# Kernel optimization log

Hardware: AMD Instinct MI355X
Metric: run time of the kernel (lower is better)

Reference implementation:

```python
import jax, jax.numpy as jnp
import numpy as np

N_NODES = 100000
N_EDGES = 6400000


def setup_inputs() -> dict:
    key = jax.random.key(0)
    k1, k2, k3, k4 = jax.random.split(key, 4)
    x = jax.random.normal(k1, (N_NODES, 1), dtype=jnp.float32)
    edge_index = jax.random.randint(k2, (2, N_EDGES), 0, N_NODES, dtype=jnp.int64)
    W1 = jax.random.normal(k3, (16, 1), dtype=jnp.float32) * 0.5
    b1 = jnp.zeros((16,), dtype=jnp.float32)
    W2 = jax.random.normal(k4, (2, 16), dtype=jnp.float32) * 0.25
    b2 = jnp.zeros((2,), dtype=jnp.float32)
    return {"x": x, "edge_index": edge_index, "W1": W1, "b1": b1, "W2": W2, "b2": b2}


def _gcn_norm(edge_index, num_nodes):
    # PyG gcn_norm with add_self_loops=True, edge_weight=1:
    # deg computed at target (col); norm = deg^-1/2[row] * deg^-1/2[col]
    loops = jnp.arange(num_nodes, dtype=edge_index.dtype)
    row = jnp.concatenate([edge_index[0], loops])
    col = jnp.concatenate([edge_index[1], loops])
    deg = jax.ops.segment_sum(jnp.ones(row.shape[0], dtype=jnp.float32), col,
                              num_segments=num_nodes)
    deg_inv_sqrt = jnp.where(deg > 0, jax.lax.rsqrt(deg), 0.0)
    norm = deg_inv_sqrt[row] * deg_inv_sqrt[col]
    return row, col, norm


def _gcn_conv(x, W, b, row, col, norm, num_nodes):
    h = x @ W.T                                   # [N, out]
    msg = norm[:, None] * h[row]                  # gather + scale, [E+N, out]
    out = jax.ops.segment_sum(msg, col, num_segments=num_nodes)  # scatter-add
    return out + b


def reference(x, edge_index, W1, b1, W2, b2):
    num_nodes = x.shape[0]
    row, col, norm = _gcn_norm(edge_index, num_nodes)
    h = _gcn_conv(x, W1, b1, row, col, norm, num_nodes)
    h = jax.nn.relu(h)
    out = _gcn_conv(h, W2, b2, row, col, norm, num_nodes)
    return out
```

## Files before the change

kernel.cpp:

```cpp
#include <hip/hip_runtime.h>
#include <cmath>


static constexpr int CSH   = 11;
static constexpr int CW    = 1 << CSH;
static constexpr int MAXNC = 64;
static constexpr int NB1   = 512;

__host__ __device__ __forceinline__ int chunk_of(int e) {
    return ((e + NB1 * 4 - 1) / (NB1 * 4)) * 4;
}

__global__ __launch_bounds__(256) void k_scatter(const int* __restrict__ row,
        const int* __restrict__ col, int* __restrict__ P1, int* __restrict__ CNT,
        int e, int NC, int PAD) {
    __shared__ int cur[MAXNC];
    const int b = blockIdx.x, tid = threadIdx.x;
    for (int j = tid; j < NC; j += 256) cur[j] = 0;
    __syncthreads();
    const int chunk = chunk_of(e);
    const int lo = b * chunk, end = min(lo + chunk, e);
    const size_t rbase = (size_t)b * NC * PAD;
    for (int i0 = lo + tid * 4; i0 + 3 < end; i0 += 1024) {
        int4 c4 = *reinterpret_cast<const int4*>(col + i0);
        int4 r4 = *reinterpret_cast<const int4*>(row + i0);
        int ca[4] = {c4.x, c4.y, c4.z, c4.w};
        int ra[4] = {r4.x, r4.y, r4.z, r4.w};
#pragma unroll
        for (int m = 0; m < 4; ++m) {
            int k = ca[m] >> CSH;
            int pos = atomicAdd(&cur[k], 1);
            if (pos < PAD)
                P1[rbase + (size_t)k * PAD + pos] = (ra[m] << CSH) | (ca[m] & (CW - 1));
        }
    }
    const int tailStart = lo + ((end - lo) & ~3);
    for (int i = tailStart + tid; i < end; i += 256) {
        int c = col[i], r = row[i];
        int k = c >> CSH;
        int pos = atomicAdd(&cur[k], 1);
        if (pos < PAD)
            P1[rbase + (size_t)k * PAD + pos] = (r << CSH) | (c & (CW - 1));
    }
    __syncthreads();
    for (int j = tid; j < NC; j += 256) CNT[b * NC + j] = min(cur[j], PAD);
}

__global__ __launch_bounds__(512) void k_deg(const int* __restrict__ P1,
        const int* __restrict__ CNT, int* __restrict__ Pd, int NC, int C, int PAD) {
    __shared__ __align__(16) int bin[CW];
    const int k = blockIdx.x / C, j = blockIdx.x % C;
    const int tid = threadIdx.x, wave = tid >> 6, lane = tid & 63;
    for (int q = tid; q < CW; q += 512) bin[q] = 0;
    __syncthreads();
    const int b0 = (j * NB1) / C, b1 = ((j + 1) * NB1) / C;
    for (int b = b0 + wave; b < b1; b += 8) {
        const int cnt = CNT[b * NC + k];
        const int* seg = P1 + ((size_t)b * NC + k) * PAD;
        const int nv = cnt & ~3;
        for (int i = lane * 4; i < nv; i += 256) {
            int4 a = *reinterpret_cast<const int4*>(seg + i);
            atomicAdd(&bin[a.x & (CW - 1)], 1); atomicAdd(&bin[a.y & (CW - 1)], 1);
            atomicAdd(&bin[a.z & (CW - 1)], 1); atomicAdd(&bin[a.w & (CW - 1)], 1);
        }
        for (int i = nv + lane; i < cnt; i += 64)
            atomicAdd(&bin[seg[i] & (CW - 1)], 1);
    }
    __syncthreads();
    int4* o4 = reinterpret_cast<int4*>(Pd + ((size_t)k * C + j) * CW);
    const int4* b4 = reinterpret_cast<const int4*>(bin);
    for (int q = tid; q < CW / 4; q += 512) o4[q] = b4[q];
}

__global__ __launch_bounds__(512) void k_aggf(const int* __restrict__ P1,
        const int* __restrict__ CNT, const float* __restrict__ src,
        float* __restrict__ Pf, int NC, int C, int PAD) {
    __shared__ __align__(16) float bin[CW];
    const int k = blockIdx.x / C, j = blockIdx.x % C;
    const int tid = threadIdx.x, wave = tid >> 6, lane = tid & 63;
    for (int q = tid; q < CW; q += 512) bin[q] = 0.0f;
    __syncthreads();
    const int b0 = (j * NB1) / C, b1 = ((j + 1) * NB1) / C;
    for (int b = b0 + wave; b < b1; b += 8) {
        const int cnt = CNT[b * NC + k];
        const int* seg = P1 + ((size_t)b * NC + k) * PAD;
        const int nv = cnt & ~3;
        for (int i = lane * 4; i < nv; i += 256) {
            int4 a = *reinterpret_cast<const int4*>(seg + i);
            float v0 = src[a.x >> CSH], v1 = src[a.y >> CSH];
            float v2 = src[a.z >> CSH], v3 = src[a.w >> CSH];
            atomicAdd(&bin[a.x & (CW - 1)], v0); atomicAdd(&bin[a.y & (CW - 1)], v1);
            atomicAdd(&bin[a.z & (CW - 1)], v2); atomicAdd(&bin[a.w & (CW - 1)], v3);
        }
        for (int i = nv + lane; i < cnt; i += 64) {
            int p = seg[i];
            atomicAdd(&bin[p & (CW - 1)], src[p >> CSH]);
        }
    }
    __syncthreads();
    float4* o4 = reinterpret_cast<float4*>(Pf + ((size_t)k * C + j) * CW);
    const float4* b4 = reinterpret_cast<const float4*>(bin);
    for (int q = tid; q < CW / 4; q += 512) o4[q] = b4[q];
}

__device__ __forceinline__ unsigned long long pack_u(float2 uv) {
    float cx = fminf(fmaxf(uv.x, -15.9f), 15.9f);
    float cy = fminf(fmaxf(uv.y, -15.9f), 15.9f);
    unsigned int tx = (unsigned int)__float2int_rn(fmaf(cx, 524288.0f, 8388608.0f));
    unsigned int ty = (unsigned int)__float2int_rn(fmaf(cy, 524288.0f, 8388608.0f));
    return ((unsigned long long)ty << 32) | tx;
}

__global__ __launch_bounds__(512) void k_agg2f(const int* __restrict__ P1,
        const int* __restrict__ CNT, const float2* __restrict__ u,
        unsigned long long* __restrict__ Pq, int NC, int C, int PAD) {
    __shared__ unsigned long long bin[CW];
    const int k = blockIdx.x / C, j = blockIdx.x % C;
    const int tid = threadIdx.x, wave = tid >> 6, lane = tid & 63;
    for (int q = tid; q < CW; q += 512) bin[q] = 0ull;
    __syncthreads();
    const int b0 = (j * NB1) / C, b1 = ((j + 1) * NB1) / C;
    for (int b = b0 + wave; b < b1; b += 8) {
        const int cnt = CNT[b * NC + k];
        const int* seg = P1 + ((size_t)b * NC + k) * PAD;
        const int nv = cnt & ~3;
        for (int i = lane * 4; i < nv; i += 256) {
            int4 a = *reinterpret_cast<const int4*>(seg + i);
            unsigned long long q0 = pack_u(u[a.x >> CSH]);
            unsigned long long q1 = pack_u(u[a.y >> CSH]);
            unsigned long long q2 = pack_u(u[a.z >> CSH]);
            unsigned long long q3 = pack_u(u[a.w >> CSH]);
            atomicAdd(&bin[a.x & (CW - 1)], q0); atomicAdd(&bin[a.y & (CW - 1)], q1);
            atomicAdd(&bin[a.z & (CW - 1)], q2); atomicAdd(&bin[a.w & (CW - 1)], q3);
        }
        for (int i = nv + lane; i < cnt; i += 64) {
            int p = seg[i];
            atomicAdd(&bin[p & (CW - 1)], pack_u(u[p >> CSH]));
        }
    }
    __syncthreads();
    unsigned long long* o = Pq + ((size_t)k * C + j) * CW;
    for (int q = tid; q < CW; q += 512) o[q] = bin[q];
}

__global__ void k_prep(const int* __restrict__ Pd, const float* __restrict__ x,
        float* __restrict__ dis, float* __restrict__ t, float* __restrict__ degf,
        int n, int C) {
    int c = blockIdx.x * blockDim.x + threadIdx.x;
    if (c >= n) return;
    int k = c >> CSH, l = c & (CW - 1);
    int d = 0;
    for (int j = 0; j < C; ++j) d += Pd[((size_t)k * C + j) * CW + l];
    degf[c] = (float)d;
    float di = rsqrtf(1.0f + (float)d);
    dis[c] = di;
    t[c] = di * x[c];
}

__global__ void k_mlp(const float* __restrict__ Pf, const float* __restrict__ dis,
        const float* __restrict__ t, const float* __restrict__ W1,
        const float* __restrict__ b1, const float* __restrict__ W2,
        float2* __restrict__ u, int n, int C) {
    int c = blockIdx.x * blockDim.x + threadIdx.x;
    if (c >= n) return;
    int k = c >> CSH, l = c & (CW - 1);
    float S = 0.0f;
    for (int j = 0; j < C; ++j) S += Pf[((size_t)k * C + j) * CW + l];
    float di = dis[c];
    float s = di * (S + t[c]);
    float a0 = 0.0f, a1 = 0.0f;
#pragma unroll
    for (int j = 0; j < 16; ++j) {
        float hh = fmaxf(fmaf(s, W1[j], b1[j]), 0.0f);
        a0 = fmaf(W2[j],      hh, a0);
        a1 = fmaf(W2[16 + j], hh, a1);
    }
    u[c] = make_float2(di * a0, di * a1);
}

__global__ void k_out(const unsigned long long* __restrict__ Pq,
        const float* __restrict__ dis, const float* __restrict__ degf,
        const float2* __restrict__ u, const float* __restrict__ b2,
        float2* __restrict__ out, int n, int C) {
    int c = blockIdx.x * blockDim.x + threadIdx.x;
    if (c >= n) return;
    int k = c >> CSH, l = c & (CW - 1);
    unsigned long long S = 0ull;
    for (int j = 0; j < C; ++j) S += Pq[((size_t)k * C + j) * CW + l];
    double dg = (double)degf[c] * 8388608.0;
    double sx = ((double)(unsigned int)(S & 0xffffffffULL) - dg) * (1.0 / 524288.0);
    double sy = ((double)(unsigned int)(S >> 32)            - dg) * (1.0 / 524288.0);
    float di = dis[c];
    float2 uc = u[c];
    out[c] = make_float2(b2[0] + di * ((float)sx + uc.x),
                         b2[1] + di * ((float)sy + uc.y));
}

__global__ void f_init_deg(float* deg, int n) {
    int i = blockIdx.x * blockDim.x + threadIdx.x;
    if (i < n) deg[i] = 1.0f;
}
__global__ void f_deg(const int* col, float* deg, int e) {
    int i = blockIdx.x * blockDim.x + threadIdx.x;
    if (i < e) atomicAdd(&deg[col[i]], 1.0f);
}
__global__ void f_dis_self(const float* x, float* deg_dis, float* s, int n) {
    int i = blockIdx.x * blockDim.x + threadIdx.x;
    if (i < n) { float di = rsqrtf(deg_dis[i]); deg_dis[i] = di; s[i] = di * di * x[i]; }
}
__global__ void f_agg1(const int* row, const int* col, const float* dis,
                       const float* x, float* s, int e) {
    int i = blockIdx.x * blockDim.x + threadIdx.x;
    if (i < e) { int r = row[i], c = col[i]; atomicAdd(&s[c], dis[r] * dis[c] * x[r]); }
}
__global__ void f_mlp(const float* s, const float* dis, const float* W1,
                      const float* b1, const float* W2, const float* b2,
                      float* h2, float* out, int n) {
    int i = blockIdx.x * blockDim.x + threadIdx.x;
    if (i < n) {
        float sv = s[i], a0 = 0.0f, a1 = 0.0f;
#pragma unroll
        for (int j = 0; j < 16; ++j) {
            float h1 = fmaxf(sv * W1[j] + b1[j], 0.0f);
            a0 = fmaf(W2[j], h1, a0); a1 = fmaf(W2[16 + j], h1, a1);
        }
        h2[2 * i] = a0; h2[2 * i + 1] = a1;
        float d2 = dis[i] * dis[i];
        out[2 * i] = b2[0] + d2 * a0; out[2 * i + 1] = b2[1] + d2 * a1;
    }
}
__global__ void f_agg2(const int* row, const int* col, const float* dis,
                       const float* h2, float* out, int e) {
    int i = blockIdx.x * blockDim.x + threadIdx.x;
    if (i < e) {
        int r = row[i], c = col[i];
        float nm = dis[r] * dis[c];
        float2 hv = *reinterpret_cast<const float2*>(&h2[2 * r]);
        atomicAdd(&out[2 * c], nm * hv.x);
        atomicAdd(&out[2 * c + 1], nm * hv.y);
    }
}

extern "C" void kernel_launch(void* const* d_in, const int* in_sizes, int n_in,
                              void* d_out, int out_size, void* d_ws, size_t ws_size,
                              hipStream_t stream) {
    const float* x  = (const float*)d_in[0];
    const int*   ei = (const int*)d_in[1];
    const float* W1 = (const float*)d_in[2];
    const float* b1 = (const float*)d_in[3];
    const float* W2 = (const float*)d_in[4];
    const float* b2 = (const float*)d_in[5];

    const int n = in_sizes[0];
    const int e = in_sizes[1] / 2;
    const int* row = ei;
    const int* col = ei + e;

    const int NC = (n + CW - 1) >> CSH;
    const size_t NCW = (size_t)NC * CW;

    const int chunk = chunk_of(e);
    const int lam = NC > 0 ? chunk / NC : 0;
    int PAD = lam + 8 * (int)std::sqrt((double)(lam > 0 ? lam : 1)) + 32;
    PAD = (PAD + 3) & ~3;

    const size_t ws4 = ws_size / 4;
    const size_t p1sz = (size_t)NB1 * NC * PAD;
    size_t base4 = p1sz + (size_t)NB1 * NC + 5ull * (size_t)n;
    base4 = (base4 + 3) & ~(size_t)3;
    long long avail = (long long)ws4 - (long long)base4;
    int Cs = (avail > 0) ? (int)min((long long)32, avail / (long long)NCW) : 0;
    int Cv = (avail > 0) ? (int)min((long long)24, avail / (long long)(2 * NCW)) : 0;

    if (NC > MAXNC || NC < 4 || Cs < 2 || Cv < 2 ||
        (long long)e > 100ll * (long long)n) {
        float* dis = (float*)d_ws; float* s = dis + n; float* h2 = s + n;
        const int gn = (n + 255) / 256, ge = (e + 255) / 256;
        f_init_deg<<<gn, 256, 0, stream>>>(dis, n);
        f_deg<<<ge, 256, 0, stream>>>(col, dis, e);
        f_dis_self<<<gn, 256, 0, stream>>>(x, dis, s, n);
        f_agg1<<<ge, 256, 0, stream>>>(row, col, dis, x, s, e);
        f_mlp<<<gn, 256, 0, stream>>>(s, dis, W1, b1, W2, b2, h2, (float*)d_out, n);
        f_agg2<<<ge, 256, 0, stream>>>(row, col, dis, h2, (float*)d_out, e);
        return;
    }

    int*    P1   = (int*)d_ws;
    int*    CNT  = P1 + p1sz;
    float*  dis  = (float*)(CNT + (size_t)NB1 * NC);
    float*  t    = dis + n;
    float*  degf = t + n;
    float2* u    = (float2*)(degf + n);
    float*  Pp   = (float*)((char*)d_ws + base4 * 4);

    const int gn = (n + 255) / 256;

    k_scatter<<<NB1, 256, 0, stream>>>(row, col, P1, CNT, e, NC, PAD);
    k_deg    <<<NC * Cs, 512, 0, stream>>>(P1, CNT, (int*)Pp, NC, Cs, PAD);
    k_prep   <<<gn, 256, 0, stream>>>((const int*)Pp, x, dis, t, degf, n, Cs);
    k_aggf   <<<NC * Cs, 512, 0, stream>>>(P1, CNT, t, Pp, NC, Cs, PAD);
    k_mlp    <<<gn, 256, 0, stream>>>(Pp, dis, t, W1, b1, W2, u, n, Cs);
    k_agg2f  <<<NC * Cv, 512, 0, stream>>>(P1, CNT, u, (unsigned long long*)Pp, NC, Cv, PAD);
    k_out    <<<gn, 256, 0, stream>>>((const unsigned long long*)Pp, dis, degf, u, b2,
                                      (float2*)d_out, n, Cv);
}
```

Measured before the change: 227.9 us.

## Build per-destination CSR-like placement once, then gather without atomics in both layers

Adds a k_place pass that bins the already-bucketed edges into a per-block, per-destination column-major slot array (with a shared overflow spill list). It also writes per-destination counts, which k_prep reuses as the degree histogram. Both aggregation layers become gather kernels: each thread owns four destinations and sums source values sequentially, replacing LDS float atomics and the fixed-point 64-bit packing with plain float sums. The cost is an extra placement pass with scattered global writes and a larger workspace. The gathers can also suffer load imbalance when destination counts vary.

```diff
diff --git a/kernel.cpp b/kernel.cpp
--- a/kernel.cpp
+++ b/kernel.cpp
@@ -6,6 +6,7 @@
 static constexpr int CW    = 1 << CSH;
 static constexpr int MAXNC = 64;
 static constexpr int NB1   = 512;
+static constexpr int SPAD  = 4096;
 
 __host__ __device__ __forceinline__ int chunk_of(int e) {
     return ((e + NB1 * 4 - 1) / (NB1 * 4)) * 4;
@@ -46,13 +47,20 @@
     for (int j = tid; j < NC; j += 256) CNT[b * NC + j] = min(cur[j], PAD);
 }
 
-__global__ __launch_bounds__(512) void k_deg(const int* __restrict__ P1,
-        const int* __restrict__ CNT, int* __restrict__ Pd, int NC, int C, int PAD) {
-    __shared__ __align__(16) int bin[CW];
+__global__ __launch_bounds__(512) void k_place(const int* __restrict__ P1,
+        const int* __restrict__ CNT, int* __restrict__ P2, int* __restrict__ CNT2,
+        int* __restrict__ SP, int* __restrict__ SPC,
+        int NC, int C, int PAD, int NPAD) {
+    __shared__ int cur[CW];
+    __shared__ int scur;
     const int k = blockIdx.x / C, j = blockIdx.x % C;
+    const size_t r = blockIdx.x;
     const int tid = threadIdx.x, wave = tid >> 6, lane = tid & 63;
-    for (int q = tid; q < CW; q += 512) bin[q] = 0;
-    __syncthreads();
+    for (int q = tid; q < CW; q += 512) cur[q] = 0;
+    if (tid == 0) scur = 0;
+    __syncthreads();
+    int* __restrict__ p2 = P2 + r * CW * (size_t)NPAD;
+    int* __restrict__ sp = SP + r * SPAD;
     const int b0 = (j * NB1) / C, b1 = ((j + 1) * NB1) / C;
     for (int b = b0 + wave; b < b1; b += 8) {
         const int cnt = CNT[b * NC + k];
@@ -60,87 +68,98 @@
         const int nv = cnt & ~3;
         for (int i = lane * 4; i < nv; i += 256) {
             int4 a = *reinterpret_cast<const int4*>(seg + i);
-            atomicAdd(&bin[a.x & (CW - 1)], 1); atomicAdd(&bin[a.y & (CW - 1)], 1);
-            atomicAdd(&bin[a.z & (CW - 1)], 1); atomicAdd(&bin[a.w & (CW - 1)], 1);
-        }
-        for (int i = nv + lane; i < cnt; i += 64)
-            atomicAdd(&bin[seg[i] & (CW - 1)], 1);
-    }
-    __syncthreads();
-    int4* o4 = reinterpret_cast<int4*>(Pd + ((size_t)k * C + j) * CW);
-    const int4* b4 = reinterpret_cast<const int4*>(bin);
-    for (int q = tid; q < CW / 4; q += 512) o4[q] = b4[q];
-}
-
-__global__ __launch_bounds__(512) void k_aggf(const int* __restrict__ P1,
-        const int* __restrict__ CNT, const float* __restrict__ src,
-        float* __restrict__ Pf, int NC, int C, int PAD) {
-    __shared__ __align__(16) float bin[CW];
-    const int k = blockIdx.x / C, j = blockIdx.x % C;
-    const int tid = threadIdx.x, wave = tid >> 6, lane = tid & 63;
-    for (int q = tid; q < CW; q += 512) bin[q] = 0.0f;
-    __syncthreads();
-    const int b0 = (j * NB1) / C, b1 = ((j + 1) * NB1) / C;
-    for (int b = b0 + wave; b < b1; b += 8) {
-        const int cnt = CNT[b * NC + k];
-        const int* seg = P1 + ((size_t)b * NC + k) * PAD;
-        const int nv = cnt & ~3;
-        for (int i = lane * 4; i < nv; i += 256) {
-            int4 a = *reinterpret_cast<const int4*>(seg + i);
-            float v0 = src[a.x >> CSH], v1 = src[a.y >> CSH];
-            float v2 = src[a.z >> CSH], v3 = src[a.w >> CSH];
-            atomicAdd(&bin[a.x & (CW - 1)], v0); atomicAdd(&bin[a.y & (CW - 1)], v1);
-            atomicAdd(&bin[a.z & (CW - 1)], v2); atomicAdd(&bin[a.w & (CW - 1)], v3);
+            int vv[4] = {a.x, a.y, a.z, a.w};
+#pragma unroll
+            for (int m = 0; m < 4; ++m) {
+                const int v = vv[m];
+                const int l = v & (CW - 1);
+                const int pos = atomicAdd(&cur[l], 1);
+                if (pos < NPAD) p2[(size_t)pos * CW + l] = v >> CSH;
+                else { int s0 = atomicAdd(&scur, 1); if (s0 < SPAD) sp[s0] = v; }
+            }
         }
         for (int i = nv + lane; i < cnt; i += 64) {
-            int p = seg[i];
-            atomicAdd(&bin[p & (CW - 1)], src[p >> CSH]);
-        }
-    }
-    __syncthreads();
-    float4* o4 = reinterpret_cast<float4*>(Pf + ((size_t)k * C + j) * CW);
-    const float4* b4 = reinterpret_cast<const float4*>(bin);
-    for (int q = tid; q < CW / 4; q += 512) o4[q] = b4[q];
-}
-
-__device__ __forceinline__ unsigned long long pack_u(float2 uv) {
-    float cx = fminf(fmaxf(uv.x, -15.9f), 15.9f);
-    float cy = fminf(fmaxf(uv.y, -15.9f), 15.9f);
-    unsigned int tx = (unsigned int)__float2int_rn(fmaf(cx, 524288.0f, 8388608.0f));
-    unsigned int ty = (unsigned int)__float2int_rn(fmaf(cy, 524288.0f, 8388608.0f));
-    return ((unsigned long long)ty << 32) | tx;
-}
-
-__global__ __launch_bounds__(512) void k_agg2f(const int* __restrict__ P1,
-        const int* __restrict__ CNT, const float2* __restrict__ u,
-        unsigned long long* __restrict__ Pq, int NC, int C, int PAD) {
-    __shared__ unsigned long long bin[CW];
-    const int k = blockIdx.x / C, j = blockIdx.x % C;
-    const int tid = threadIdx.x, wave = tid >> 6, lane = tid & 63;
-    for (int q = tid; q < CW; q += 512) bin[q] = 0ull;
-    __syncthreads();
-    const int b0 = (j * NB1) / C, b1 = ((j + 1) * NB1) / C;
-    for (int b = b0 + wave; b < b1; b += 8) {
-        const int cnt = CNT[b * NC + k];
-        const int* seg = P1 + ((size_t)b * NC + k) * PAD;
-        const int nv = cnt & ~3;
-        for (int i = lane * 4; i < nv; i += 256) {
-            int4 a = *reinterpret_cast<const int4*>(seg + i);
-            unsigned long long q0 = pack_u(u[a.x >> CSH]);
-            unsigned long long q1 = pack_u(u[a.y >> CSH]);
-            unsigned long long q2 = pack_u(u[a.z >> CSH]);
-            unsigned long long q3 = pack_u(u[a.w >> CSH]);
-            atomicAdd(&bin[a.x & (CW - 1)], q0); atomicAdd(&bin[a.y & (CW - 1)], q1);
-            atomicAdd(&bin[a.z & (CW - 1)], q2); atomicAdd(&bin[a.w & (CW - 1)], q3);
-        }
-        for (int i = nv + lane; i < cnt; i += 64) {
-            int p = seg[i];
-            atomicAdd(&bin[p & (CW - 1)], pack_u(u[p >> CSH]));
-        }
-    }
-    __syncthreads();
-    unsigned long long* o = Pq + ((size_t)k * C + j) * CW;
-    for (int q = tid; q < CW; q += 512) o[q] = bin[q];
+            const int v = seg[i];
+            const int l = v & (CW - 1);
+            const int pos = atomicAdd(&cur[l], 1);
+            if (pos < NPAD) p2[(size_t)pos * CW + l] = v >> CSH;
+            else { int s0 = atomicAdd(&scur, 1); if (s0 < SPAD) sp[s0] = v; }
+        }
+    }
+    __syncthreads();
+    for (int q = tid; q < CW; q += 512) CNT2[r * CW + q] = cur[q];
+    if (tid == 0) SPC[r] = min(scur, SPAD);
+}
+
+__global__ __launch_bounds__(512) void k_gath1(const int* __restrict__ P2,
+        const int* __restrict__ CNT2, const int* __restrict__ SP,
+        const int* __restrict__ SPC, const float* __restrict__ t,
+        float* __restrict__ Pf, int NPAD) {
+    __shared__ float sbin[CW];
+    const size_t r = blockIdx.x;
+    const int tid = threadIdx.x;
+    for (int q = tid; q < CW; q += 512) sbin[q] = 0.0f;
+    __syncthreads();
+    const int spc = SPC[r];
+    for (int i = tid; i < spc; i += 512) {
+        const int v = SP[r * SPAD + i];
+        atomicAdd(&sbin[v & (CW - 1)], t[v >> CSH]);
+    }
+    __syncthreads();
+    const int* __restrict__ p2 = P2 + r * CW * (size_t)NPAD;
+    const int* __restrict__ cc = CNT2 + r * CW;
+    const int l0 = tid, l1 = tid + 512, l2 = tid + 1024, l3 = tid + 1536;
+    const int c0 = min(cc[l0], NPAD), c1 = min(cc[l1], NPAD);
+    const int c2 = min(cc[l2], NPAD), c3 = min(cc[l3], NPAD);
+    float S0 = sbin[l0], S1 = sbin[l1], S2 = sbin[l2], S3 = sbin[l3];
+    const int cm = max(max(c0, c1), max(c2, c3));
+    for (int p = 0; p < cm; ++p) {
+        const int* rp = p2 + (size_t)p * CW;
+        if (p < c0) S0 += t[rp[l0]];
+        if (p < c1) S1 += t[rp[l1]];
+        if (p < c2) S2 += t[rp[l2]];
+        if (p < c3) S3 += t[rp[l3]];
+    }
+    float* o = Pf + r * CW;
+    o[l0] = S0; o[l1] = S1; o[l2] = S2; o[l3] = S3;
+}
+
+__global__ __launch_bounds__(512) void k_gath2(const int* __restrict__ P2,
+        const int* __restrict__ CNT2, const int* __restrict__ SP,
+        const int* __restrict__ SPC, const float2* __restrict__ u,
+        float2* __restrict__ Pf2, int NPAD) {
+    __shared__ float sbx[CW];
+    __shared__ float sby[CW];
+    const size_t r = blockIdx.x;
+    const int tid = threadIdx.x;
+    for (int q = tid; q < CW; q += 512) { sbx[q] = 0.0f; sby[q] = 0.0f; }
+    __syncthreads();
+    const int spc = SPC[r];
+    for (int i = tid; i < spc; i += 512) {
+        const int v = SP[r * SPAD + i];
+        float2 uv = u[v >> CSH];
+        atomicAdd(&sbx[v & (CW - 1)], uv.x);
+        atomicAdd(&sby[v & (CW - 1)], uv.y);
+    }
+    __syncthreads();
+    const int* __restrict__ p2 = P2 + r * CW * (size_t)NPAD;
+    const int* __restrict__ cc = CNT2 + r * CW;
+    const int l0 = tid, l1 = tid + 512, l2 = tid + 1024, l3 = tid + 1536;
+    const int c0 = min(cc[l0], NPAD), c1 = min(cc[l1], NPAD);
+    const int c2 = min(cc[l2], NPAD), c3 = min(cc[l3], NPAD);
+    float S0x = sbx[l0], S1x = sbx[l1], S2x = sbx[l2], S3x = sbx[l3];
+    float S0y = sby[l0], S1y = sby[l1], S2y = sby[l2], S3y = sby[l3];
+    const int cm = max(max(c0, c1), max(c2, c3));
+    for (int p = 0; p < cm; ++p) {
+        const int* rp = p2 + (size_t)p * CW;
+        if (p < c0) { float2 v = u[rp[l0]]; S0x += v.x; S0y += v.y; }
+        if (p < c1) { float2 v = u[rp[l1]]; S1x += v.x; S1y += v.y; }
+        if (p < c2) { float2 v = u[rp[l2]]; S2x += v.x; S2y += v.y; }
+        if (p < c3) { float2 v = u[rp[l3]]; S3x += v.x; S3y += v.y; }
+    }
+    float2* o = Pf2 + r * CW;
+    o[l0] = make_float2(S0x, S0y); o[l1] = make_float2(S1x, S1y);
+    o[l2] = make_float2(S2x, S2y); o[l3] = make_float2(S3x, S3y);
 }
 
 __global__ void k_prep(const int* __restrict__ Pd, const float* __restrict__ x,
@@ -178,6 +197,120 @@
     u[c] = make_float2(di * a0, di * a1);
 }
 
+__global__ void k_out2(const float2* __restrict__ Pf2, const float* __restrict__ dis,
+        const float2* __restrict__ u, const float* __restrict__ b2,
+        float2* __restrict__ out, int n, int C) {
+    int c = blockIdx.x * blockDim.x + threadIdx.x;
+    if (c >= n) return;
+    int k = c >> CSH, l = c & (CW - 1);
+    float sx = 0.0f, sy = 0.0f;
+    for (int j = 0; j < C; ++j) {
+        float2 p = Pf2[((size_t)k * C + j) * CW + l];
+        sx += p.x; sy += p.y;
+    }
+    float di = dis[c];
+    float2 uc = u[c];
+    out[c] = make_float2(b2[0] + di * (sx + uc.x),
+                         b2[1] + di * (sy + uc.y));
+}
+
+__global__ __launch_bounds__(512) void k_deg(const int* __restrict__ P1,
+        const int* __restrict__ CNT, int* __restrict__ Pd, int NC, int C, int PAD) {
+    __shared__ __align__(16) int bin[CW];
+    const int k = blockIdx.x / C, j = blockIdx.x % C;
+    const int tid = threadIdx.x, wave = tid >> 6, lane = tid & 63;
+    for (int q = tid; q < CW; q += 512) bin[q] = 0;
+    __syncthreads();
+    const int b0 = (j * NB1) / C, b1 = ((j + 1) * NB1) / C;
+    for (int b = b0 + wave; b < b1; b += 8) {
+        const int cnt = CNT[b * NC + k];
+        const int* seg = P1 + ((size_t)b * NC + k) * PAD;
+        const int nv = cnt & ~3;
+        for (int i = lane * 4; i < nv; i += 256) {
+            int4 a = *reinterpret_cast<const int4*>(seg + i);
+            atomicAdd(&bin[a.x & (CW - 1)], 1); atomicAdd(&bin[a.y & (CW - 1)], 1);
+            atomicAdd(&bin[a.z & (CW - 1)], 1); atomicAdd(&bin[a.w & (CW - 1)], 1);
+        }
+        for (int i = nv + lane; i < cnt; i += 64)
+            atomicAdd(&bin[seg[i] & (CW - 1)], 1);
+    }
+    __syncthreads();
+    int4* o4 = reinterpret_cast<int4*>(Pd + ((size_t)k * C + j) * CW);
+    const int4* b4 = reinterpret_cast<const int4*>(bin);
+    for (int q = tid; q < CW / 4; q += 512) o4[q] = b4[q];
+}
+
+__global__ __launch_bounds__(512) void k_aggf(const int* __restrict__ P1,
+        const int* __restrict__ CNT, const float* __restrict__ src,
+        float* __restrict__ Pf, int NC, int C, int PAD) {
+    __shared__ __align__(16) float bin[CW];
+    const int k = blockIdx.x / C, j = blockIdx.x % C;
+    const int tid = threadIdx.x, wave = tid >> 6, lane = tid & 63;
+    for (int q = tid; q < CW; q += 512) bin[q] = 0.0f;
+    __syncthreads();
+    const int b0 = (j * NB1) / C, b1 = ((j + 1) * NB1) / C;
+    for (int b = b0 + wave; b < b1; b += 8) {
+        const int cnt = CNT[b * NC + k];
+        const int* seg = P1 + ((size_t)b * NC + k) * PAD;
+        const int nv = cnt & ~3;
+        for (int i = lane * 4; i < nv; i += 256) {
+            int4 a = *reinterpret_cast<const int4*>(seg + i);
+            float v0 = src[a.x >> CSH], v1 = src[a.y >> CSH];
+            float v2 = src[a.z >> CSH], v3 = src[a.w >> CSH];
+            atomicAdd(&bin[a.x & (CW - 1)], v0); atomicAdd(&bin[a.y & (CW - 1)], v1);
+            atomicAdd(&bin[a.z & (CW - 1)], v2); atomicAdd(&bin[a.w & (CW - 1)], v3);
+        }
+        for (int i = nv + lane; i < cnt; i += 64) {
+            int p = seg[i];
+            atomicAdd(&bin[p & (CW - 1)], src[p >> CSH]);
+        }
+    }
+    __syncthreads();
+    float4* o4 = reinterpret_cast<float4*>(Pf + ((size_t)k * C + j) * CW);
+    const float4* b4 = reinterpret_cast<const float4*>(bin);
+    for (int q = tid; q < CW / 4; q += 512) o4[q] = b4[q];
+}
+
+__device__ __forceinline__ unsigned long long pack_u(float2 uv) {
+    float cx = fminf(fmaxf(uv.x, -15.9f), 15.9f);
+    float cy = fminf(fmaxf(uv.y, -15.9f), 15.9f);
+    unsigned int tx = (unsigned int)__float2int_rn(fmaf(cx, 524288.0f, 8388608.0f));
+    unsigned int ty = (unsigned int)__float2int_rn(fmaf(cy, 524288.0f, 8388608.0f));
+    return ((unsigned long long)ty << 32) | tx;
+}
+
+__global__ __launch_bounds__(512) void k_agg2f(const int* __restrict__ P1,
+        const int* __restrict__ CNT, const float2* __restrict__ u,
+        unsigned long long* __restrict__ Pq, int NC, int C, int PAD) {
+    __shared__ unsigned long long bin[CW];
+    const int k = blockIdx.x / C, j = blockIdx.x % C;
+    const int tid = threadIdx.x, wave = tid >> 6, lane = tid & 63;
+    for (int q = tid; q < CW; q += 512) bin[q] = 0ull;
+    __syncthreads();
+    const int b0 = (j * NB1) / C, b1 = ((j + 1) * NB1) / C;
+    for (int b = b0 + wave; b < b1; b += 8) {
+        const int cnt = CNT[b * NC + k];
+        const int* seg = P1 + ((size_t)b * NC + k) * PAD;
+        const int nv = cnt & ~3;
+        for (int i = lane * 4; i < nv; i += 256) {
+            int4 a = *reinterpret_cast<const int4*>(seg + i);
+            unsigned long long q0 = pack_u(u[a.x >> CSH]);
+            unsigned long long q1 = pack_u(u[a.y >> CSH]);
+            unsigned long long q2 = pack_u(u[a.z >> CSH]);
+            unsigned long long q3 = pack_u(u[a.w >> CSH]);
+            atomicAdd(&bin[a.x & (CW - 1)], q0); atomicAdd(&bin[a.y & (CW - 1)], q1);
+            atomicAdd(&bin[a.z & (CW - 1)], q2); atomicAdd(&bin[a.w & (CW - 1)], q3);
+        }
+        for (int i = nv + lane; i < cnt; i += 64) {
+            int p = seg[i];
+            atomicAdd(&bin[p & (CW - 1)], pack_u(u[p >> CSH]));
+        }
+    }
+    __syncthreads();
+    unsigned long long* o = Pq + ((size_t)k * C + j) * CW;
+    for (int q = tid; q < CW; q += 512) o[q] = bin[q];
+}
+
 __global__ void k_out(const unsigned long long* __restrict__ Pq,
         const float* __restrict__ dis, const float* __restrict__ degf,
         const float2* __restrict__ u, const float* __restrict__ b2,
@@ -258,14 +391,62 @@
 
     const int NC = (n + CW - 1) >> CSH;
     const size_t NCW = (size_t)NC * CW;
+    const size_t ws4 = ws_size / 4;
 
     const int chunk = chunk_of(e);
     const int lam = NC > 0 ? chunk / NC : 0;
     int PAD = lam + 8 * (int)std::sqrt((double)(lam > 0 ? lam : 1)) + 32;
     PAD = (PAD + 3) & ~3;
-
-    const size_t ws4 = ws_size / 4;
     const size_t p1sz = (size_t)NB1 * NC * PAD;
+    const int gn = (n + 255) / 256;
+
+    if (NC <= MAXNC && NC >= 4 && e > 0) {
+        const int C2 = 10;
+        const size_t cells = (size_t)NC * C2 * CW;
+        const double lm = (double)e / (double)cells;
+        if (lm <= 32.0) {
+            const int na = (n + 3) & ~3;
+            const size_t fixed4 = p1sz + (size_t)NB1 * NC + 5ull * (size_t)na;
+            int cand[3];
+            cand[0] = (int)std::ceil(lm + 2.5 * std::sqrt(lm) + 6.0);
+            cand[1] = (int)std::ceil(lm + 1.2 * std::sqrt(lm) + 2.0);
+            cand[2] = (int)std::ceil(lm + 0.5 * std::sqrt(lm));
+            for (int ci = 0; ci < 3; ++ci) {
+                const int NPAD = cand[ci] > 4 ? cand[ci] : 4;
+                const size_t need = fixed4
+                                  + cells
+                                  + (size_t)NC * C2 + 64
+                                  + (size_t)NC * C2 * SPAD
+                                  + cells * (size_t)NPAD;
+                if (need > ws4 || p1sz < cells * 3) continue;
+
+                int*    P1   = (int*)d_ws;
+                int*    CNT  = P1 + p1sz;
+                float*  dis  = (float*)(CNT + (size_t)NB1 * NC);
+                float*  t    = dis + na;
+                float*  degf = t + na;
+                float2* u    = (float2*)(degf + na);
+                int*    CNT2 = (int*)d_ws + fixed4;
+                int*    SPC  = CNT2 + cells;
+                int*    SP   = SPC + (size_t)NC * C2 + 64;
+                int*    P2   = SP + (size_t)NC * C2 * SPAD;
+                float*  Pf   = (float*)P1;
+                float2* Pf2  = (float2*)(P1 + cells);
+
+                k_scatter<<<NB1, 256, 0, stream>>>(row, col, P1, CNT, e, NC, PAD);
+                k_place  <<<NC * C2, 512, 0, stream>>>(P1, CNT, P2, CNT2, SP, SPC,
+                                                       NC, C2, PAD, NPAD);
+                k_prep   <<<gn, 256, 0, stream>>>(CNT2, x, dis, t, degf, n, C2);
+                k_gath1  <<<NC * C2, 512, 0, stream>>>(P2, CNT2, SP, SPC, t, Pf, NPAD);
+                k_mlp    <<<gn, 256, 0, stream>>>(Pf, dis, t, W1, b1, W2, u, n, C2);
+                k_gath2  <<<NC * C2, 512, 0, stream>>>(P2, CNT2, SP, SPC, u, Pf2, NPAD);
+                k_out2   <<<gn, 256, 0, stream>>>(Pf2, dis, u, b2,
+                                                  (float2*)d_out, n, C2);
+                return;
+            }
+        }
+    }
+
     size_t base4 = p1sz + (size_t)NB1 * NC + 5ull * (size_t)n;
     base4 = (base4 + 3) & ~(size_t)3;
     long long avail = (long long)ws4 - (long long)base4;
@@ -275,7 +456,7 @@
     if (NC > MAXNC || NC < 4 || Cs < 2 || Cv < 2 ||
         (long long)e > 100ll * (long long)n) {
         float* dis = (float*)d_ws; float* s = dis + n; float* h2 = s + n;
-        const int gn = (n + 255) / 256, ge = (e + 255) / 256;
+        const int ge = (e + 255) / 256;
         f_init_deg<<<gn, 256, 0, stream>>>(dis, n);
         f_deg<<<ge, 256, 0, stream>>>(col, dis, e);
         f_dis_self<<<gn, 256, 0, stream>>>(x, dis, s, n);
@@ -292,8 +473,6 @@
     float*  degf = t + n;
     float2* u    = (float2*)(degf + n);
     float*  Pp   = (float*)((char*)d_ws + base4 * 4);
-
-    const int gn = (n + 255) / 256;
 
     k_scatter<<<NB1, 256, 0, stream>>>(row, col, P1, CNT, e, NC, PAD);
     k_deg    <<<NC * Cs, 512, 0, stream>>>(P1, CNT, (int*)Pp, NC, Cs, PAD);
```

Result: slower. 272.5 us (+19.6%).

## Fuse seven pipeline kernels into one cooperative persistent kernel with grid syncs

Applied to the files above, without the earlier changes.

Replaces the seven separate launches (scatter, degree count, prep, first aggregation, MLP, second aggregation, output) with one cooperative kernel of NB1 blocks that runs each stage in turn, separated by grid.sync. Work is distributed with grid-stride job loops. The aim is to cut per-kernel launch gaps and tail drain between the short stages. In exchange, blocks now use 512 threads and a shared bin sized for the largest stage, which may reduce occupancy. Grid-wide barriers are costly and all 512 blocks must be co-resident, otherwise the code falls back to the separate launches.

```diff
diff --git a/kernel.cpp b/kernel.cpp
--- a/kernel.cpp
+++ b/kernel.cpp
@@ -1,5 +1,8 @@
 #include <hip/hip_runtime.h>
+#include <hip/hip_cooperative_groups.h>
 #include <cmath>
+
+namespace cg = cooperative_groups;
 
 
 static constexpr int CSH   = 11;
@@ -9,6 +12,208 @@
 
 __host__ __device__ __forceinline__ int chunk_of(int e) {
     return ((e + NB1 * 4 - 1) / (NB1 * 4)) * 4;
+}
+
+__device__ __forceinline__ unsigned long long pack_u(float2 uv) {
+    float cx = fminf(fmaxf(uv.x, -15.9f), 15.9f);
+    float cy = fminf(fmaxf(uv.y, -15.9f), 15.9f);
+    unsigned int tx = (unsigned int)__float2int_rn(fmaf(cx, 524288.0f, 8388608.0f));
+    unsigned int ty = (unsigned int)__float2int_rn(fmaf(cy, 524288.0f, 8388608.0f));
+    return ((unsigned long long)ty << 32) | tx;
+}
+
+__global__ __launch_bounds__(512, 4) void k_fused(
+        const int* __restrict__ row, const int* __restrict__ col,
+        const float* __restrict__ x,  const float* __restrict__ W1,
+        const float* __restrict__ b1, const float* __restrict__ W2,
+        const float* __restrict__ b2,
+        int* __restrict__ P1, int* __restrict__ CNT,
+        float* __restrict__ dis, float* __restrict__ t,
+        float* __restrict__ degf, float2* __restrict__ u,
+        float* __restrict__ Pp, float2* __restrict__ out,
+        int n, int e, int NC, int PAD, int Cs, int Cv) {
+    cg::grid_group grid = cg::this_grid();
+    __shared__ __align__(16) unsigned long long binU[CW];
+    __shared__ int cur[MAXNC];
+    int*   binI = (int*)binU;
+    float* binF = (float*)binU;
+    const int tid = threadIdx.x, wave = tid >> 6, lane = tid & 63;
+
+    {
+        const int b = blockIdx.x;
+        for (int j = tid; j < NC; j += 512) cur[j] = 0;
+        __syncthreads();
+        const int chunk = chunk_of(e);
+        const int lo = b * chunk, end = min(lo + chunk, e);
+        const size_t rbase = (size_t)b * NC * PAD;
+        for (int i0 = lo + tid * 4; i0 + 3 < end; i0 += 2048) {
+            int4 c4 = *reinterpret_cast<const int4*>(col + i0);
+            int4 r4 = *reinterpret_cast<const int4*>(row + i0);
+            int ca[4] = {c4.x, c4.y, c4.z, c4.w};
+            int ra[4] = {r4.x, r4.y, r4.z, r4.w};
+#pragma unroll
+            for (int m = 0; m < 4; ++m) {
+                int k = ca[m] >> CSH;
+                int pos = atomicAdd(&cur[k], 1);
+                if (pos < PAD)
+                    P1[rbase + (size_t)k * PAD + pos] =
+                        (ra[m] << CSH) | (ca[m] & (CW - 1));
+            }
+        }
+        const int tailStart = lo + ((end - lo) & ~3);
+        for (int i = tailStart + tid; i < end; i += 512) {
+            int c = col[i], r = row[i];
+            int k = c >> CSH;
+            int pos = atomicAdd(&cur[k], 1);
+            if (pos < PAD)
+                P1[rbase + (size_t)k * PAD + pos] = (r << CSH) | (c & (CW - 1));
+        }
+        __syncthreads();
+        for (int j = tid; j < NC; j += 512) CNT[b * NC + j] = min(cur[j], PAD);
+    }
+    grid.sync();
+
+    {
+        int* Pd = (int*)Pp;
+        for (int job = blockIdx.x; job < NC * Cs; job += NB1) {
+            const int k = job / Cs, j = job % Cs;
+            for (int q = tid; q < CW; q += 512) binI[q] = 0;
+            __syncthreads();
+            const int b0 = (j * NB1) / Cs, b1e = ((j + 1) * NB1) / Cs;
+            for (int b = b0 + wave; b < b1e; b += 8) {
+                const int cnt = CNT[b * NC + k];
+                const int* seg = P1 + ((size_t)b * NC + k) * PAD;
+                const int nv = cnt & ~3;
+                for (int i = lane * 4; i < nv; i += 256) {
+                    int4 a = *reinterpret_cast<const int4*>(seg + i);
+                    atomicAdd(&binI[a.x & (CW - 1)], 1);
+                    atomicAdd(&binI[a.y & (CW - 1)], 1);
+                    atomicAdd(&binI[a.z & (CW - 1)], 1);
+                    atomicAdd(&binI[a.w & (CW - 1)], 1);
+                }
+                for (int i = nv + lane; i < cnt; i += 64)
+                    atomicAdd(&binI[seg[i] & (CW - 1)], 1);
+            }
+            __syncthreads();
+            for (int q = tid; q < CW; q += 512)
+                Pd[((size_t)k * Cs + j) * CW + q] = binI[q];
+        }
+    }
+    grid.sync();
+
+    {
+        const int* Pd = (const int*)Pp;
+        for (int c = blockIdx.x * 512 + tid; c < n; c += NB1 * 512) {
+            int k = c >> CSH, l = c & (CW - 1);
+            int d = 0;
+            for (int j = 0; j < Cs; ++j) d += Pd[((size_t)k * Cs + j) * CW + l];
+            degf[c] = (float)d;
+            float di = rsqrtf(1.0f + (float)d);
+            dis[c] = di;
+            t[c] = di * x[c];
+        }
+    }
+    grid.sync();
+
+    {
+        for (int job = blockIdx.x; job < NC * Cs; job += NB1) {
+            const int k = job / Cs, j = job % Cs;
+            for (int q = tid; q < CW; q += 512) binF[q] = 0.0f;
+            __syncthreads();
+            const int b0 = (j * NB1) / Cs, b1e = ((j + 1) * NB1) / Cs;
+            for (int b = b0 + wave; b < b1e; b += 8) {
+                const int cnt = CNT[b * NC + k];
+                const int* seg = P1 + ((size_t)b * NC + k) * PAD;
+                const int nv = cnt & ~3;
+                for (int i = lane * 4; i < nv; i += 256) {
+                    int4 a = *reinterpret_cast<const int4*>(seg + i);
+                    float v0 = t[a.x >> CSH], v1 = t[a.y >> CSH];
+                    float v2 = t[a.z >> CSH], v3 = t[a.w >> CSH];
+                    atomicAdd(&binF[a.x & (CW - 1)], v0);
+                    atomicAdd(&binF[a.y & (CW - 1)], v1);
+                    atomicAdd(&binF[a.z & (CW - 1)], v2);
+                    atomicAdd(&binF[a.w & (CW - 1)], v3);
+                }
+                for (int i = nv + lane; i < cnt; i += 64) {
+                    int p = seg[i];
+                    atomicAdd(&binF[p & (CW - 1)], t[p >> CSH]);
+                }
+            }
+            __syncthreads();
+            for (int q = tid; q < CW; q += 512)
+                Pp[((size_t)k * Cs + j) * CW + q] = binF[q];
+        }
+    }
+    grid.sync();
+
+    {
+        for (int c = blockIdx.x * 512 + tid; c < n; c += NB1 * 512) {
+            int k = c >> CSH, l = c & (CW - 1);
+            float S = 0.0f;
+            for (int j = 0; j < Cs; ++j) S += Pp[((size_t)k * Cs + j) * CW + l];
+            float di = dis[c];
+            float s = di * (S + t[c]);
+            float a0 = 0.0f, a1 = 0.0f;
+#pragma unroll
+            for (int j = 0; j < 16; ++j) {
+                float hh = fmaxf(fmaf(s, W1[j], b1[j]), 0.0f);
+                a0 = fmaf(W2[j],      hh, a0);
+                a1 = fmaf(W2[16 + j], hh, a1);
+            }
+            u[c] = make_float2(di * a0, di * a1);
+        }
+    }
+    grid.sync();
+
+    {
+        unsigned long long* Pq = (unsigned long long*)Pp;
+        for (int job = blockIdx.x; job < NC * Cv; job += NB1) {
+            const int k = job / Cv, j = job % Cv;
+            for (int q = tid; q < CW; q += 512) binU[q] = 0ull;
+            __syncthreads();
+            const int b0 = (j * NB1) / Cv, b1e = ((j + 1) * NB1) / Cv;
+            for (int b = b0 + wave; b < b1e; b += 8) {
+                const int cnt = CNT[b * NC + k];
+                const int* seg = P1 + ((size_t)b * NC + k) * PAD;
+                const int nv = cnt & ~3;
+                for (int i = lane * 4; i < nv; i += 256) {
+                    int4 a = *reinterpret_cast<const int4*>(seg + i);
+                    unsigned long long q0 = pack_u(u[a.x >> CSH]);
+                    unsigned long long q1 = pack_u(u[a.y >> CSH]);
+                    unsigned long long q2 = pack_u(u[a.z >> CSH]);
+                    unsigned long long q3 = pack_u(u[a.w >> CSH]);
+                    atomicAdd(&binU[a.x & (CW - 1)], q0);
+                    atomicAdd(&binU[a.y & (CW - 1)], q1);
+                    atomicAdd(&binU[a.z & (CW - 1)], q2);
+                    atomicAdd(&binU[a.w & (CW - 1)], q3);
+                }
+                for (int i = nv + lane; i < cnt; i += 64) {
+                    int p = seg[i];
+                    atomicAdd(&binU[p & (CW - 1)], pack_u(u[p >> CSH]));
+                }
+            }
+            __syncthreads();
+            for (int q = tid; q < CW; q += 512)
+                Pq[((size_t)k * Cv + j) * CW + q] = binU[q];
+        }
+    }
+    grid.sync();
+
+    {
+        const unsigned long long* Pq = (const unsigned long long*)Pp;
+        for (int c = blockIdx.x * 512 + tid; c < n; c += NB1 * 512) {
+            int k = c >> CSH, l = c & (CW - 1);
+            unsigned long long S = 0ull;
+            for (int j = 0; j < Cv; ++j) S += Pq[((size_t)k * Cv + j) * CW + l];
+            double dg = (double)degf[c] * 8388608.0;
+            double sx = ((double)(unsigned int)(S & 0xffffffffULL) - dg) * (1.0 / 524288.0);
+            double sy = ((double)(unsigned int)(S >> 32)            - dg) * (1.0 / 524288.0);
+            float di = dis[c];
+            float2 uc = u[c];
+            out[c] = make_float2(b2[0] + di * ((float)sx + uc.x),
+                                 b2[1] + di * ((float)sy + uc.y));
+        }
+    }
 }
 
 __global__ __launch_bounds__(256) void k_scatter(const int* __restrict__ row,
@@ -101,14 +306,6 @@
     float4* o4 = reinterpret_cast<float4*>(Pf + ((size_t)k * C + j) * CW);
     const float4* b4 = reinterpret_cast<const float4*>(bin);
     for (int q = tid; q < CW / 4; q += 512) o4[q] = b4[q];
-}
-
-__device__ __forceinline__ unsigned long long pack_u(float2 uv) {
-    float cx = fminf(fmaxf(uv.x, -15.9f), 15.9f);
-    float cy = fminf(fmaxf(uv.y, -15.9f), 15.9f);
-    unsigned int tx = (unsigned int)__float2int_rn(fmaf(cx, 524288.0f, 8388608.0f));
-    unsigned int ty = (unsigned int)__float2int_rn(fmaf(cy, 524288.0f, 8388608.0f));
-    return ((unsigned long long)ty << 32) | tx;
 }
 
 __global__ __launch_bounds__(512) void k_agg2f(const int* __restrict__ P1,
@@ -272,10 +469,11 @@
     int Cs = (avail > 0) ? (int)min((long long)32, avail / (long long)NCW) : 0;
     int Cv = (avail > 0) ? (int)min((long long)24, avail / (long long)(2 * NCW)) : 0;
 
+    const int gn = (n + 255) / 256;
     if (NC > MAXNC || NC < 4 || Cs < 2 || Cv < 2 ||
         (long long)e > 100ll * (long long)n) {
         float* dis = (float*)d_ws; float* s = dis + n; float* h2 = s + n;
-        const int gn = (n + 255) / 256, ge = (e + 255) / 256;
+        const int ge = (e + 255) / 256;
         f_init_deg<<<gn, 256, 0, stream>>>(dis, n);
         f_deg<<<ge, 256, 0, stream>>>(col, dis, e);
         f_dis_self<<<gn, 256, 0, stream>>>(x, dis, s, n);
@@ -292,8 +490,28 @@
     float*  degf = t + n;
     float2* u    = (float2*)(degf + n);
     float*  Pp   = (float*)((char*)d_ws + base4 * 4);
-
-    const int gn = (n + 255) / 256;
+    float2* outp = (float2*)d_out;
+
+    static int coop_ok = -1;
+    if (coop_ok < 0) {
+        int dev = 0, attr = 0, mab = 0;
+        hipGetDevice(&dev);
+        hipDeviceGetAttribute(&attr, hipDeviceAttributeCooperativeLaunch, dev);
+        hipOccupancyMaxActiveBlocksPerMultiprocessor(&mab, k_fused, 512, 0);
+        coop_ok = (attr != 0 && mab >= 2) ? 1 : 0;
+    }
+    if (coop_ok == 1) {
+        int en = e, nn = n, ncc = NC, pad = PAD, cs = Cs, cv = Cv;
+        void* args[] = { (void*)&row, (void*)&col, (void*)&x, (void*)&W1,
+                         (void*)&b1, (void*)&W2, (void*)&b2, (void*)&P1,
+                         (void*)&CNT, (void*)&dis, (void*)&t, (void*)&degf,
+                         (void*)&u, (void*)&Pp, (void*)&outp,
+                         (void*)&nn, (void*)&en, (void*)&ncc, (void*)&pad,
+                         (void*)&cs, (void*)&cv };
+        hipError_t rc = hipLaunchCooperativeKernel(k_fused, dim3(NB1), dim3(512),
+                                                   args, 0, stream);
+        if (rc == hipSuccess) return;
+    }
 
     k_scatter<<<NB1, 256, 0, stream>>>(row, col, P1, CNT, e, NC, PAD);
     k_deg    <<<NC * Cs, 512, 0, stream>>>(P1, CNT, (int*)Pp, NC, Cs, PAD);
```

After: 644.0 us. 183% more time.
